# Performance work log

Measured on AMD Instinct MI355X. Metric: run time of the kernel, lower is better.

Reference implementation:

```python
import jax, jax.numpy as jnp
import numpy as np

B, S, D = 4, 4096, 1024

def setup_inputs() -> dict:
    key = jax.random.key(0)
    k1, k2, k3 = jax.random.split(key, 3)
    x = jax.random.normal(k1, (B, S, D), dtype=jnp.float32)
    # torch nn.Linear weights: [out_features, in_features], scaled for sanity
    W_qkv = jax.random.normal(k2, (3 * D, D), dtype=jnp.float32) * (1.0 / np.sqrt(D))
    W_o = jax.random.normal(k3, (D, D), dtype=jnp.float32) * (1.0 / np.sqrt(D))
    return {"x": x, "W_qkv": W_qkv, "W_o": W_o}


def reference(x, W_qkv, W_o):
    d_model = x.shape[-1]
    # torch Linear: y = x @ W.T
    qkv = jnp.einsum("bsd,ed->bse", x, W_qkv)  # [B, S, 3D]
    Q, K, V = jnp.split(qkv, 3, axis=-1)
    scale = 1.0 / jnp.sqrt(jnp.asarray(d_model, dtype=x.dtype))
    logits = jnp.einsum("bqd,bkd->bqk", Q, K) * scale  # [B, S, S]
    weights = jax.nn.softmax(logits, axis=-1)
    attn = jnp.einsum("bqk,bkd->bqd", weights, V)  # [B, S, D]
    out = jnp.einsum("bsd,ed->bse", attn, W_o)  # [B, S, D]
    return out
```

## Files before the change

kernel.cpp:

```cpp
#include <hip/hip_runtime.h>
#include <hip/hip_bf16.h>
#include <stdint.h>

typedef unsigned short u16;
typedef __bf16 bf16x8 __attribute__((ext_vector_type(8)));
typedef unsigned short u16x8 __attribute__((ext_vector_type(8)));
typedef float f32x4 __attribute__((ext_vector_type(4)));

__device__ __forceinline__ float bf2f(u16 h) {
  union { uint32_t u; float f; } x;
  x.u = ((uint32_t)h) << 16;
  return x.f;
}
__device__ __forceinline__ u16 f2bf(float f) {
  union { float f; uint32_t u; } x;
  x.f = f;
  uint32_t r = x.u + 0x7FFFu + ((x.u >> 16) & 1u);
  return (u16)(r >> 16);
}

__device__ __forceinline__ void gload_lds16(const u16* g, u16* l) {
  __builtin_amdgcn_global_load_lds(
      (const __attribute__((address_space(1))) uint32_t*)g,
      (__attribute__((address_space(3))) uint32_t*)l, 16, 0, 0);
}

typedef __attribute__((address_space(3))) const u16 lds_cu16;
template <int OFF>
__device__ __forceinline__ f32x4 ds_read128o(const lds_cu16* p) {
  f32x4 r;
  asm volatile("ds_read_b128 %0, %1 offset:%2" : "=v"(r) : "v"(p), "n"(OFF));
  return r;
}

__global__ __launch_bounds__(256) void cvt_all(
    const float* __restrict__ x, const float* __restrict__ w1,
    const float* __restrict__ w2, u16* __restrict__ xb,
    u16* __restrict__ w1b, u16* __restrict__ w2b, int n1, int n2, int n3) {
  int i = blockIdx.x * 256 + threadIdx.x;
  const float* src;
  u16* dst;
  int j = i;
  if (i < n1) { src = x; dst = xb; }
  else if (i < n1 + n2) { src = w1; dst = w1b; j = i - n1; }
  else if (i < n1 + n2 + n3) { src = w2; dst = w2b; j = i - n1 - n2; }
  else return;
  const float4* p = (const float4*)src + (size_t)j * 2;
  float4 a = p[0], b = p[1];
  u16x8 o;
  o[0] = f2bf(a.x); o[1] = f2bf(a.y); o[2] = f2bf(a.z); o[3] = f2bf(a.w);
  o[4] = f2bf(b.x); o[5] = f2bf(b.y); o[6] = f2bf(b.z); o[7] = f2bf(b.w);
  ((u16x8*)dst)[j] = o;
}

template <typename OT, int EPI>
__global__ __launch_bounds__(256) void gemm_bt(
    const u16* __restrict__ A, int lda, long zsA,
    const u16* __restrict__ B, int ldb, long zsB,
    OT* __restrict__ C, int ldc, long zsC,
    int K, float scale, const float* __restrict__ rs) {
  const int z = blockIdx.z;
  A += (long)z * zsA;
  B += (long)z * zsB;
  C += (long)z * zsC;
  if constexpr (EPI == 2) rs += (long)z * 4096;

  __shared__ __align__(16) u16 As[2 * 128 * 32];
  __shared__ __align__(16) u16 Bs[2 * 128 * 32];
  const int tid  = threadIdx.x;
  const int m0   = blockIdx.y * 128;
  const int n0   = blockIdx.x * 128;
  const int wave = tid >> 6;
  const int lane = tid & 63;
  const int wm   = (wave >> 1) * 64;
  const int wn   = (wave & 1) * 64;
  const int l15  = lane & 15;
  const int quad = lane >> 4;

  f32x4 acc[4][4];
#pragma unroll
  for (int i = 0; i < 4; ++i)
#pragma unroll
    for (int j = 0; j < 4; ++j) acc[i][j] = f32x4{0.f, 0.f, 0.f, 0.f};

  const u16* gA0 = A + (size_t)(m0 + (tid >> 2)) * lda + (tid & 3) * 8;
  const u16* gA1 = A + (size_t)(m0 + 64 + (tid >> 2)) * lda + (tid & 3) * 8;
  const u16* gB0 = B + (size_t)(n0 + (tid >> 2)) * ldb + (tid & 3) * 8;
  const u16* gB1 = B + (size_t)(n0 + 64 + (tid >> 2)) * ldb + (tid & 3) * 8;
  u16* lA0 = As + tid * 8;
  u16* lA1 = As + (256 + tid) * 8;
  u16* lB0 = Bs + tid * 8;
  u16* lB1 = Bs + (256 + tid) * 8;

  for (int k0 = 0; k0 < K; k0 += 64) {
    __syncthreads();
#pragma unroll
    for (int s = 0; s < 2; ++s) {
      gload_lds16(gA0 + k0 + s * 32, lA0 + s * 4096);
      gload_lds16(gA1 + k0 + s * 32, lA1 + s * 4096);
      gload_lds16(gB0 + k0 + s * 32, lB0 + s * 4096);
      gload_lds16(gB1 + k0 + s * 32, lB1 + s * 4096);
    }
    __syncthreads();

#pragma unroll
    for (int s = 0; s < 2; ++s) {
      u16x8 a[4], b[4];
#pragma unroll
      for (int i = 0; i < 4; ++i)
        a[i] = *(const u16x8*)(As + s * 4096 + (wm + i * 16 + l15) * 32 + quad * 8);
#pragma unroll
      for (int j = 0; j < 4; ++j)
        b[j] = *(const u16x8*)(Bs + s * 4096 + (wn + j * 16 + l15) * 32 + quad * 8);
#pragma unroll
      for (int i = 0; i < 4; ++i)
#pragma unroll
        for (int j = 0; j < 4; ++j)
          acc[i][j] = __builtin_amdgcn_mfma_f32_16x16x32_bf16(
              __builtin_bit_cast(bf16x8, a[i]), __builtin_bit_cast(bf16x8, b[j]),
              acc[i][j], 0, 0, 0);
    }
  }

#pragma unroll
  for (int i = 0; i < 4; ++i) {
#pragma unroll
    for (int r = 0; r < 4; ++r) {
      const int row = m0 + wm + i * 16 + quad * 4 + r;
      float mul = scale;
      if constexpr (EPI == 2) mul = scale / rs[row];
      const size_t ro = (size_t)row * ldc;
#pragma unroll
      for (int j = 0; j < 4; ++j) {
        float v = acc[i][j][r] * mul;
        if constexpr (EPI == 1) v = __expf(v);
        const int col = n0 + wn + j * 16 + l15;
        if constexpr (__is_same(OT, float))
          C[ro + col] = v;
        else
          C[ro + col] = f2bf(v);
      }
    }
  }
}

#define BAR() __builtin_amdgcn_s_barrier()
#define PRIO(n) __builtin_amdgcn_s_setprio(n)
#define WAITV(n) asm volatile("s_waitcnt vmcnt(" #n ")")
#define WAITLGKM() asm volatile("s_waitcnt lgkmcnt(0)")
#define SCHEDB() __builtin_amdgcn_sched_barrier(0)
#define DSR(p, off) ds_read128o<(off)>(p)
#define AO(qm, ii, kk) ((((qm) * 4 + (ii)) * 2 + (kk)) * 1024)
#define BO(qn, jj, kk) ((((qn) * 2 + (jj)) * 2 + (kk)) * 1024)

#define STG(c, h, q, t)                                                         \
  gload_lds16(((h) < 2 ? gAs : gBs) +                                           \
                  (size_t)(((h) & 1) * 128 + (q) * 64) * ((h) < 2 ? lda : ldb) + \
                  (size_t)(t) * 64,                                             \
              lds + (c) * 32768 + ((h) < 2 ? 0 : 16384) +                       \
                  (((h) & 1) * 8 + (q) * 4) * 1024 + wsub * 512)

#define MM(qm, ii, qn, jj, AV, BV)                                              \
  acc[(qm) * 4 + (ii)][(qn) * 2 + (jj)] =                                       \
      __builtin_amdgcn_mfma_f32_16x16x32_bf16(                                  \
          __builtin_bit_cast(bf16x8, AV), __builtin_bit_cast(bf16x8, BV),       \
          acc[(qm) * 4 + (ii)][(qn) * 2 + (jj)], 0, 0, 0);

#define PH(LA, LB, qm, qn, STGS, TAILW)                                         \
  {                                                                             \
    f32x4 a0k0 = DSR(LA, AO(qm, 0, 0)), a0k1 = DSR(LA, AO(qm, 0, 1));           \
    f32x4 a1k0 = DSR(LA, AO(qm, 1, 0)), a1k1 = DSR(LA, AO(qm, 1, 1));           \
    f32x4 a2k0 = DSR(LA, AO(qm, 2, 0)), a2k1 = DSR(LA, AO(qm, 2, 1));           \
    f32x4 a3k0 = DSR(LA, AO(qm, 3, 0)), a3k1 = DSR(LA, AO(qm, 3, 1));           \
    f32x4 b0k0 = DSR(LB, BO(qn, 0, 0)), b0k1 = DSR(LB, BO(qn, 0, 1));           \
    f32x4 b1k0 = DSR(LB, BO(qn, 1, 0)), b1k1 = DSR(LB, BO(qn, 1, 1));           \
    STGS                                                                        \
    BAR();                                                                      \
    WAITLGKM();                                                                 \
    SCHEDB();                                                                   \
    PRIO(1);                                                                    \
    MM(qm, 0, qn, 0, a0k0, b0k0) MM(qm, 0, qn, 1, a0k0, b1k0)                   \
    MM(qm, 1, qn, 0, a1k0, b0k0) MM(qm, 1, qn, 1, a1k0, b1k0)                   \
    MM(qm, 2, qn, 0, a2k0, b0k0) MM(qm, 2, qn, 1, a2k0, b1k0)                   \
    MM(qm, 3, qn, 0, a3k0, b0k0) MM(qm, 3, qn, 1, a3k0, b1k0)                   \
    MM(qm, 0, qn, 0, a0k1, b0k1) MM(qm, 0, qn, 1, a0k1, b1k1)                   \
    MM(qm, 1, qn, 0, a1k1, b0k1) MM(qm, 1, qn, 1, a1k1, b1k1)                   \
    MM(qm, 2, qn, 0, a2k1, b0k1) MM(qm, 2, qn, 1, a2k1, b1k1)                   \
    MM(qm, 3, qn, 0, a3k1, b0k1) MM(qm, 3, qn, 1, a3k1, b1k1)                   \
    PRIO(0);                                                                    \
    SCHEDB();                                                                   \
    TAILW                                                                       \
    BAR();                                                                      \
  }

template <typename OT, int EPI>
__global__ __launch_bounds__(512, 2) void gemm256(
    const u16* __restrict__ A, int lda, long zsA,
    const u16* __restrict__ B, int ldb, long zsB,
    OT* __restrict__ C, int ldc, long zsC,
    int K, float scale, const float* __restrict__ rs) {
  __shared__ __align__(16) u16 lds[65536];
  const int z = blockIdx.z;
  A += (long)z * zsA;
  B += (long)z * zsB;
  C += (long)z * zsC;
  if constexpr (EPI == 2) rs += (long)z * 4096;

  const int tid  = threadIdx.x;
  const int lane = tid & 63;
  const int w    = tid >> 6;
  const int wm   = w >> 2;
  const int wn   = w & 3;
  const int wm8  = wm * 8;
  const int wn4  = wn * 4;
  const int l15  = lane & 15;
  const int quad = lane >> 4;
  const int m0   = blockIdx.y * 256;
  const int n0   = blockIdx.x * 256;

  const int srow = (w >> 1) * 16 + (lane >> 2);
  const int kcol = ((lane & 3) * 8) ^ ((lane & 32) ? 16 : 0);
  const int skb  = w & 1;
  const u16* gAs = A + (size_t)(m0 + srow) * lda + skb * 32 + kcol;
  const u16* gBs = B + (size_t)(n0 + srow) * ldb + skb * 32 + kcol;
  const int wsub = (w >> 1) * 2 + skb;

  const int rq = (l15 * 32 + quad * 8) ^ ((l15 & 8) << 1);
  const lds_cu16* Lp  = (const lds_cu16*)lds;
  const lds_cu16* LA0 = Lp + wm8 * 1024 + rq;
  const lds_cu16* LA1 = LA0 + 32768;
  const lds_cu16* LB0 = Lp + 16384 + wn4 * 1024 + rq;
  const lds_cu16* LB1 = LB0 + 32768;

  f32x4 acc[8][4];
#pragma unroll
  for (int i = 0; i < 8; ++i)
#pragma unroll
    for (int j = 0; j < 4; ++j) acc[i][j] = f32x4{0.f, 0.f, 0.f, 0.f};

  const int ni = K >> 7;

#pragma unroll
  for (int h = 0; h < 4; ++h) { STG(0, h, 0, 0); STG(0, h, 1, 0); }
  WAITV(0);
  BAR();

  for (int i = 0; i < ni; ++i) {
    const int t1 = 2 * i + 1, t2 = 2 * i + 2;
    const bool more = (i + 1 < ni);

    PH(LA0, LB0, 0, 0,
       STG(1, 0, 0, t1); STG(1, 0, 1, t1); STG(1, 1, 0, t1); STG(1, 1, 1, t1);, )
    PH(LA0, LB0, 0, 1,
       STG(1, 2, 0, t1); STG(1, 2, 1, t1); STG(1, 3, 0, t1); STG(1, 3, 1, t1);, )
    PH(LA0, LB0, 1, 0, , )
    PH(LA0, LB0, 1, 1, , WAITV(0);)
    PH(LA1, LB1, 0, 0,
       if (more) { STG(0, 0, 0, t2); STG(0, 0, 1, t2);
                   STG(0, 1, 0, t2); STG(0, 1, 1, t2); }, )
    PH(LA1, LB1, 0, 1,
       if (more) { STG(0, 2, 0, t2); STG(0, 2, 1, t2);
                   STG(0, 3, 0, t2); STG(0, 3, 1, t2); }, )
    PH(LA1, LB1, 1, 0, , )
    PH(LA1, LB1, 1, 1, , WAITV(0);)
  }

#pragma unroll
  for (int i = 0; i < 8; ++i) {
#pragma unroll
    for (int r = 0; r < 4; ++r) {
      const int row = m0 + wm * 128 + i * 16 + quad * 4 + r;
      float mul = scale;
      if constexpr (EPI == 2) mul = scale / rs[row];
      const size_t ro = (size_t)row * ldc;
#pragma unroll
      for (int j = 0; j < 4; ++j) {
        float v = acc[i][j][r] * mul;
        if constexpr (EPI == 1) v = __expf(v);
        const int col = n0 + wn * 64 + j * 16 + l15;
        if constexpr (__is_same(OT, float))
          C[ro + col] = v;
        else
          C[ro + col] = f2bf(v);
      }
    }
  }
}

__global__ __launch_bounds__(256) void rowsum_rows(
    const u16* __restrict__ P, long zsP, float* __restrict__ rs) {
  const int row = blockIdx.x;
  const int z   = blockIdx.y;
  const u16* p = P + (long)z * zsP + (size_t)row * 4096;
  const int tid  = threadIdx.x;
  const int lane = tid & 63;
  const int wave = tid >> 6;

  u16x8 h0 = *(const u16x8*)(p + tid * 16);
  u16x8 h1 = *(const u16x8*)(p + tid * 16 + 8);
  float s = 0.f;
#pragma unroll
  for (int j = 0; j < 8; ++j) s += bf2f(h0[j]) + bf2f(h1[j]);
  for (int o = 32; o > 0; o >>= 1) s += __shfl_xor(s, o, 64);
  __shared__ float red[4];
  if (lane == 0) red[wave] = s;
  __syncthreads();
  if (tid == 0) rs[(size_t)z * 4096 + row] = red[0] + red[1] + red[2] + red[3];
}

__global__ __launch_bounds__(256) void transpose_v(
    const u16* __restrict__ V, int ldv, long zsV,
    u16* __restrict__ Vt, int ldt, long zsT) {
  const int z = blockIdx.z;
  V  += (long)z * zsV;
  Vt += (long)z * zsT;
  __shared__ u16 T[64][65];
  const int d0 = blockIdx.x * 64;
  const int s0 = blockIdx.y * 64;
  const int tid = threadIdx.x;
  const int c = tid & 63;
  const int rbase = (tid >> 6) * 16;
#pragma unroll
  for (int r = 0; r < 16; ++r)
    T[rbase + r][c] = V[(size_t)(s0 + rbase + r) * ldv + d0 + c];
  __syncthreads();
#pragma unroll
  for (int r = 0; r < 16; ++r)
    Vt[(size_t)(d0 + rbase + r) * ldt + s0 + c] = T[c][rbase + r];
}

extern "C" void kernel_launch(void* const* d_in, const int* in_sizes, int n_in,
                              void* d_out, int out_size, void* d_ws, size_t ws_size,
                              hipStream_t stream) {
  const float* x    = (const float*)d_in[0];
  const float* Wqkv = (const float*)d_in[1];
  const float* Wo   = (const float*)d_in[2];
  float* out = (float*)d_out;

  const int Bn = 4, S = 4096, D = 1024;
  const int M = Bn * S;
  const int E = 3 * D;
  const long SE = (long)S * E, SS = (long)S * S, DS = (long)D * S, SD = (long)S * D;

  const int nz = (ws_size >= (size_t)226492416) ? 2 : 1;

  char* ws = (char*)d_ws;
  size_t off = 0;
  u16* qkv = (u16*)(ws + off);  off += (size_t)M * E * 2;
  u16* Sb  = (u16*)(ws + off);  off += (size_t)nz * S * S * 2;
  u16* Vt  = (u16*)(ws + off);  off += (size_t)nz * D * S * 2;
  u16* xb  = (u16*)(ws + off);  off += (size_t)M * D * 2;
  u16* attn = xb;
  u16* Wqkvb = (u16*)(ws + off); off += (size_t)E * D * 2;
  u16* Wob   = (u16*)(ws + off); off += (size_t)D * D * 2;
  float* rs = (float*)Wqkvb;

  const int n1 = M * D / 8, n2 = E * D / 8, n3 = D * D / 8;
  cvt_all<<<(n1 + n2 + n3 + 255) / 256, 256, 0, stream>>>(
      x, Wqkv, Wo, xb, Wqkvb, Wob, n1, n2, n3);

  gemm256<u16, 0><<<dim3(E / 256, M / 256, 1), 512, 0, stream>>>(
      xb, D, 0, Wqkvb, D, 0, qkv, E, 0, D, 1.0f, nullptr);

  const float scl = 0.03125f;
  for (int c = 0; c < Bn; c += nz) {
    const u16* Qc = qkv + (size_t)c * SE;
    transpose_v<<<dim3(D / 64, S / 64, nz), 256, 0, stream>>>(
        Qc + 2 * D, E, SE, Vt, S, DS);
    gemm256<u16, 1><<<dim3(S / 256, S / 256, nz), 512, 0, stream>>>(
        Qc, E, SE, Qc + D, E, SE, Sb, S, SS, D, scl, nullptr);
    rowsum_rows<<<dim3(S, nz), 256, 0, stream>>>(Sb, SS, rs);
    gemm_bt<u16, 2><<<dim3(D / 128, S / 128, nz), 256, 0, stream>>>(
        Sb, S, SS, Vt, S, DS, attn + (size_t)c * SD, D, SD, S, 1.0f, rs);
  }

  gemm256<float, 0><<<dim3(D / 256, M / 256, 1), 512, 0, stream>>>(
      attn, D, 0, Wob, D, 0, out, D, 0, D, 1.0f, nullptr);
}
```

Before: 629.8 us.

## Reschedule 256x256 GEMM mainloop with fragment reuse and deeper partial-wait prefetch

Restructures the GEMM main loop so each wave keeps A/B fragments in registers across phases, reusing A fragments over two B sub-tiles and skipping redundant LDS reads in one phase. Global-to-LDS staging is interleaved one tile further ahead with partial vmcnt waits instead of full drains, and a peeled final iteration replaces the per-iteration 'more' check. The wave-to-output mapping is changed to interleaved 64/32-row/col blocks so the register reuse matches. This adds register pressure and a fragile hand-tuned wait/barrier schedule.

After: 628.6 us. Within noise of the previous version (-0.2%).

```diff
diff --git a/kernel.cpp b/kernel.cpp
--- a/kernel.cpp
+++ b/kernel.cpp
@@ -149,9 +149,6 @@
 #define WAITV(n) asm volatile("s_waitcnt vmcnt(" #n ")")
 #define WAITLGKM() asm volatile("s_waitcnt lgkmcnt(0)")
 #define SCHEDB() __builtin_amdgcn_sched_barrier(0)
-#define DSR(p, off) ds_read128o<(off)>(p)
-#define AO(qm, ii, kk) ((((qm) * 4 + (ii)) * 2 + (kk)) * 1024)
-#define BO(qn, jj, kk) ((((qn) * 2 + (jj)) * 2 + (kk)) * 1024)
 
 #define STG(c, h, q, t)                                                         \
   gload_lds16(((h) < 2 ? gAs : gBs) +                                           \
@@ -160,38 +157,40 @@
               lds + (c) * 32768 + ((h) < 2 ? 0 : 16384) +                       \
                   (((h) & 1) * 8 + (q) * 4) * 1024 + wsub * 512)
 
-#define MM(qm, ii, qn, jj, AV, BV)                                              \
-  acc[(qm) * 4 + (ii)][(qn) * 2 + (jj)] =                                       \
-      __builtin_amdgcn_mfma_f32_16x16x32_bf16(                                  \
-          __builtin_bit_cast(bf16x8, AV), __builtin_bit_cast(bf16x8, BV),       \
-          acc[(qm) * 4 + (ii)][(qn) * 2 + (jj)], 0, 0, 0);
-
-#define PH(LA, LB, qm, qn, STGS, TAILW)                                         \
-  {                                                                             \
-    f32x4 a0k0 = DSR(LA, AO(qm, 0, 0)), a0k1 = DSR(LA, AO(qm, 0, 1));           \
-    f32x4 a1k0 = DSR(LA, AO(qm, 1, 0)), a1k1 = DSR(LA, AO(qm, 1, 1));           \
-    f32x4 a2k0 = DSR(LA, AO(qm, 2, 0)), a2k1 = DSR(LA, AO(qm, 2, 1));           \
-    f32x4 a3k0 = DSR(LA, AO(qm, 3, 0)), a3k1 = DSR(LA, AO(qm, 3, 1));           \
-    f32x4 b0k0 = DSR(LB, BO(qn, 0, 0)), b0k1 = DSR(LB, BO(qn, 0, 1));           \
-    f32x4 b1k0 = DSR(LB, BO(qn, 1, 0)), b1k1 = DSR(LB, BO(qn, 1, 1));           \
-    STGS                                                                        \
-    BAR();                                                                      \
-    WAITLGKM();                                                                 \
-    SCHEDB();                                                                   \
-    PRIO(1);                                                                    \
-    MM(qm, 0, qn, 0, a0k0, b0k0) MM(qm, 0, qn, 1, a0k0, b1k0)                   \
-    MM(qm, 1, qn, 0, a1k0, b0k0) MM(qm, 1, qn, 1, a1k0, b1k0)                   \
-    MM(qm, 2, qn, 0, a2k0, b0k0) MM(qm, 2, qn, 1, a2k0, b1k0)                   \
-    MM(qm, 3, qn, 0, a3k0, b0k0) MM(qm, 3, qn, 1, a3k0, b1k0)                   \
-    MM(qm, 0, qn, 0, a0k1, b0k1) MM(qm, 0, qn, 1, a0k1, b1k1)                   \
-    MM(qm, 1, qn, 0, a1k1, b0k1) MM(qm, 1, qn, 1, a1k1, b1k1)                   \
-    MM(qm, 2, qn, 0, a2k1, b0k1) MM(qm, 2, qn, 1, a2k1, b1k1)                   \
-    MM(qm, 3, qn, 0, a3k1, b0k1) MM(qm, 3, qn, 1, a3k1, b1k1)                   \
-    PRIO(0);                                                                    \
-    SCHEDB();                                                                   \
-    TAILW                                                                       \
-    BAR();                                                                      \
-  }
+#define RDA(dst, base, RB8)                                                     \
+  dst[0] = ds_read128o<(((RB8) + 0) * 2048 + 0)>(base);                         \
+  dst[1] = ds_read128o<(((RB8) + 0) * 2048 + 1024)>(base);                      \
+  dst[2] = ds_read128o<(((RB8) + 1) * 2048 + 0)>(base);                         \
+  dst[3] = ds_read128o<(((RB8) + 1) * 2048 + 1024)>(base);                      \
+  dst[4] = ds_read128o<(((RB8) + 2) * 2048 + 0)>(base);                         \
+  dst[5] = ds_read128o<(((RB8) + 2) * 2048 + 1024)>(base);                      \
+  dst[6] = ds_read128o<(((RB8) + 3) * 2048 + 0)>(base);                         \
+  dst[7] = ds_read128o<(((RB8) + 3) * 2048 + 1024)>(base);
+
+#define RDB(dst, base, RB8)                                                     \
+  dst[0] = ds_read128o<(((RB8) + 0) * 2048 + 0)>(base);                         \
+  dst[1] = ds_read128o<(((RB8) + 0) * 2048 + 1024)>(base);                      \
+  dst[2] = ds_read128o<(((RB8) + 1) * 2048 + 0)>(base);                         \
+  dst[3] = ds_read128o<(((RB8) + 1) * 2048 + 1024)>(base);
+
+#define MM1(i, j, AV, BV)                                                       \
+  acc[i][j] = __builtin_amdgcn_mfma_f32_16x16x32_bf16(                          \
+      __builtin_bit_cast(bf16x8, AV), __builtin_bit_cast(bf16x8, BV),           \
+      acc[i][j], 0, 0, 0);
+
+#define MFMA16(qm, qn, FA, FB)                                                  \
+  PRIO(1);                                                                      \
+  MM1((qm)*4+0, (qn)*2+0, FA[0], FB[0]) MM1((qm)*4+0, (qn)*2+1, FA[0], FB[2])   \
+  MM1((qm)*4+1, (qn)*2+0, FA[2], FB[0]) MM1((qm)*4+1, (qn)*2+1, FA[2], FB[2])   \
+  MM1((qm)*4+2, (qn)*2+0, FA[4], FB[0]) MM1((qm)*4+2, (qn)*2+1, FA[4], FB[2])   \
+  MM1((qm)*4+3, (qn)*2+0, FA[6], FB[0]) MM1((qm)*4+3, (qn)*2+1, FA[6], FB[2])   \
+  MM1((qm)*4+0, (qn)*2+0, FA[1], FB[1]) MM1((qm)*4+0, (qn)*2+1, FA[1], FB[3])   \
+  MM1((qm)*4+1, (qn)*2+0, FA[3], FB[1]) MM1((qm)*4+1, (qn)*2+1, FA[3], FB[3])   \
+  MM1((qm)*4+2, (qn)*2+0, FA[5], FB[1]) MM1((qm)*4+2, (qn)*2+1, FA[5], FB[3])   \
+  MM1((qm)*4+3, (qn)*2+0, FA[7], FB[1]) MM1((qm)*4+3, (qn)*2+1, FA[7], FB[3])   \
+  PRIO(0);
+
+#define PH_MID() SCHEDB(); BAR(); WAITLGKM(); SCHEDB()
 
 template <typename OT, int EPI>
 __global__ __launch_bounds__(512, 2) void gemm256(
@@ -211,8 +210,6 @@
   const int w    = tid >> 6;
   const int wm   = w >> 2;
   const int wn   = w & 3;
-  const int wm8  = wm * 8;
-  const int wn4  = wn * 4;
   const int l15  = lane & 15;
   const int quad = lane >> 4;
   const int m0   = blockIdx.y * 256;
@@ -227,9 +224,9 @@
 
   const int rq = (l15 * 32 + quad * 8) ^ ((l15 & 8) << 1);
   const lds_cu16* Lp  = (const lds_cu16*)lds;
-  const lds_cu16* LA0 = Lp + wm8 * 1024 + rq;
+  const lds_cu16* LA0 = Lp + wm * 4 * 1024 + rq;
   const lds_cu16* LA1 = LA0 + 32768;
-  const lds_cu16* LB0 = Lp + 16384 + wn4 * 1024 + rq;
+  const lds_cu16* LB0 = Lp + 16384 + wn * 2 * 1024 + rq;
   const lds_cu16* LB1 = LB0 + 32768;
 
   f32x4 acc[8][4];
@@ -237,39 +234,70 @@
   for (int i = 0; i < 8; ++i)
 #pragma unroll
     for (int j = 0; j < 4; ++j) acc[i][j] = f32x4{0.f, 0.f, 0.f, 0.f};
+  f32x4 fA0[8], fA1[8], fB0[4], fB1[4];
 
   const int ni = K >> 7;
 
-#pragma unroll
-  for (int h = 0; h < 4; ++h) { STG(0, h, 0, 0); STG(0, h, 1, 0); }
-  WAITV(0);
+  STG(0, 0, 0, 0); STG(0, 0, 1, 0);
+  STG(0, 2, 0, 0); STG(0, 2, 1, 0);
+  STG(0, 3, 0, 0); STG(0, 3, 1, 0);
+  STG(0, 1, 0, 0); STG(0, 1, 1, 0);
+  STG(1, 0, 0, 1); STG(1, 0, 1, 1);
+  STG(1, 3, 0, 1); STG(1, 3, 1, 1);
+  STG(1, 2, 0, 1); STG(1, 2, 1, 1);
+  WAITV(6);
   BAR();
 
-  for (int i = 0; i < ni; ++i) {
-    const int t1 = 2 * i + 1, t2 = 2 * i + 2;
-    const bool more = (i + 1 < ni);
-
-    PH(LA0, LB0, 0, 0,
-       STG(1, 0, 0, t1); STG(1, 0, 1, t1); STG(1, 1, 0, t1); STG(1, 1, 1, t1);, )
-    PH(LA0, LB0, 0, 1,
-       STG(1, 2, 0, t1); STG(1, 2, 1, t1); STG(1, 3, 0, t1); STG(1, 3, 1, t1);, )
-    PH(LA0, LB0, 1, 0, , )
-    PH(LA0, LB0, 1, 1, , WAITV(0);)
-    PH(LA1, LB1, 0, 0,
-       if (more) { STG(0, 0, 0, t2); STG(0, 0, 1, t2);
-                   STG(0, 1, 0, t2); STG(0, 1, 1, t2); }, )
-    PH(LA1, LB1, 0, 1,
-       if (more) { STG(0, 2, 0, t2); STG(0, 2, 1, t2);
-                   STG(0, 3, 0, t2); STG(0, 3, 1, t2); }, )
-    PH(LA1, LB1, 1, 0, , )
-    PH(LA1, LB1, 1, 1, , WAITV(0);)
+  for (int i = 0; i < ni - 1; ++i) {
+    const int t1 = 2 * i + 1, t2 = 2 * i + 2, t3 = 2 * i + 3;
+    RDA(fA0, LA0, 0) RDB(fB0, LB0, 0)
+    STG(1, 1, 0, t1); STG(1, 1, 1, t1);
+    PH_MID(); MFMA16(0, 0, fA0, fB0) SCHEDB(); WAITV(6); BAR();
+    RDB(fB1, LB0, 8)
+    STG(0, 0, 0, t2); STG(0, 0, 1, t2);
+    PH_MID(); MFMA16(0, 1, fA0, fB1) SCHEDB(); WAITV(6); BAR();
+    RDA(fA1, LA0, 8) RDB(fB0, LB0, 0)
+    STG(0, 3, 0, t2); STG(0, 3, 1, t2);
+    PH_MID(); MFMA16(1, 0, fA1, fB0) SCHEDB(); WAITV(6); BAR();
+    STG(0, 2, 0, t2); STG(0, 2, 1, t2);
+    SCHEDB(); BAR(); SCHEDB(); MFMA16(1, 1, fA1, fB1) SCHEDB(); WAITV(6); BAR();
+    RDA(fA0, LA1, 0) RDB(fB0, LB1, 0)
+    STG(0, 1, 0, t2); STG(0, 1, 1, t2);
+    PH_MID(); MFMA16(0, 0, fA0, fB0) SCHEDB(); WAITV(6); BAR();
+    RDB(fB1, LB1, 8)
+    STG(1, 0, 0, t3); STG(1, 0, 1, t3);
+    PH_MID(); MFMA16(0, 1, fA0, fB1) SCHEDB(); WAITV(6); BAR();
+    RDA(fA1, LA1, 8) RDB(fB0, LB1, 0)
+    STG(1, 3, 0, t3); STG(1, 3, 1, t3);
+    PH_MID(); MFMA16(1, 0, fA1, fB0) SCHEDB(); WAITV(6); BAR();
+    STG(1, 2, 0, t3); STG(1, 2, 1, t3);
+    SCHEDB(); BAR(); SCHEDB(); MFMA16(1, 1, fA1, fB1) SCHEDB(); WAITV(6); BAR();
+  }
+
+  {
+    const int t1 = 2 * ni - 1;
+    RDA(fA0, LA0, 0) RDB(fB0, LB0, 0)
+    STG(1, 1, 0, t1); STG(1, 1, 1, t1);
+    PH_MID(); MFMA16(0, 0, fA0, fB0) SCHEDB(); WAITV(6); BAR();
+    RDB(fB1, LB0, 8)
+    PH_MID(); MFMA16(0, 1, fA0, fB1) SCHEDB(); WAITV(4); BAR();
+    RDA(fA1, LA0, 8) RDB(fB0, LB0, 0)
+    PH_MID(); MFMA16(1, 0, fA1, fB0) SCHEDB(); WAITV(2); BAR();
+    SCHEDB(); BAR(); SCHEDB(); MFMA16(1, 1, fA1, fB1) SCHEDB(); WAITV(0); BAR();
+    RDA(fA0, LA1, 0) RDB(fB0, LB1, 0)
+    PH_MID(); MFMA16(0, 0, fA0, fB0) SCHEDB(); BAR();
+    RDB(fB1, LB1, 8)
+    PH_MID(); MFMA16(0, 1, fA0, fB1) SCHEDB(); BAR();
+    RDA(fA1, LA1, 8) RDB(fB0, LB1, 0)
+    PH_MID(); MFMA16(1, 0, fA1, fB0) SCHEDB(); BAR();
+    WAITLGKM(); SCHEDB(); MFMA16(1, 1, fA1, fB1)
   }
 
 #pragma unroll
   for (int i = 0; i < 8; ++i) {
 #pragma unroll
     for (int r = 0; r < 4; ++r) {
-      const int row = m0 + wm * 128 + i * 16 + quad * 4 + r;
+      const int row = m0 + (i >> 2) * 128 + wm * 64 + (i & 3) * 16 + quad * 4 + r;
       float mul = scale;
       if constexpr (EPI == 2) mul = scale / rs[row];
       const size_t ro = (size_t)row * ldc;
@@ -277,7 +305,7 @@
       for (int j = 0; j < 4; ++j) {
         float v = acc[i][j][r] * mul;
         if constexpr (EPI == 1) v = __expf(v);
-        const int col = n0 + wn * 64 + j * 16 + l15;
+        const int col = n0 + (j >> 1) * 128 + wn * 32 + (j & 1) * 16 + l15;
         if constexpr (__is_same(OT, float))
           C[ro + col] = v;
         else
```
